# Kernel optimization log

Measured on AMD Instinct MI355X. Metric: run time of the kernel, lower is better.

## Reference

```python
import jax, jax.numpy as jnp
import numpy as np

TAU = 0.02
M = 5  # len(modality_types) + 1; modality 0 == padding


def setup_inputs() -> dict:
    B, Q, S, D = 64, 32, 256, 128
    key = jax.random.key(0)
    k0, k1, k2, k3, k4 = jax.random.split(key, 5)
    q = jax.random.normal(k0, (B, Q, D), dtype=jnp.float32)
    q = q / jnp.linalg.norm(q, axis=-1, keepdims=True)
    d = jax.random.normal(k1, (B, S, D), dtype=jnp.float32)
    d = d / jnp.linalg.norm(d, axis=-1, keepdims=True)
    # guarantee every modality 0..M-1 appears in each doc (first M tokens)
    head = jnp.tile(jnp.arange(M, dtype=jnp.int32), (B, 1))
    rest = jax.random.randint(k2, (B, S - M), 0, M, dtype=jnp.int32)
    modality_ids = jnp.concatenate([head, rest], axis=1)
    query_types = jax.random.randint(k3, (B,), 1, M, dtype=jnp.int32)  # in [1, M-1]
    lengths = jax.random.randint(k4, (B,), Q // 2, Q + 1)
    query_mask = jnp.arange(Q)[None, :] < lengths[:, None]
    return {"query_emb": q, "doc_emb": d, "modality_ids": modality_ids,
            "query_types": query_types, "query_mask": query_mask}


def _loss(query_emb, doc_emb, modality_ids, query_types, query_mask):
    B = query_emb.shape[0]
    idx = jnp.arange(B)
    # token-level similarity: (B, C, Q, S)
    base = jnp.einsum('bqd,csd->bcqs', query_emb, doc_emb)
    qnorm = jnp.maximum(query_mask.sum(axis=1), 1).astype(base.dtype)  # (B,)

    # agg (ColBERT max-sim): max over non-pad doc tokens, masked query sum
    nonpad = (modality_ids != 0)[None, :, None, :]
    agg_max = jnp.where(nonpad, base, -jnp.inf).max(axis=-1)           # (B, C, Q)
    sim = (agg_max * query_mask[:, None, :].astype(base.dtype)).sum(axis=-1)
    sim = sim / qnorm[:, None]                                          # (B, C)

    # _all_modality_sims: segmented max over s per modality, then sum over q
    per_mod = []
    for m in range(M):
        mask_m = (modality_ids == m)[None, :, None, :]
        per_mod.append(jnp.where(mask_m, base, -jnp.inf).max(axis=-1).sum(axis=-1))
    sims = jnp.stack(per_mod, axis=-1)                                  # (B, C, M)
    sims = sims / qnorm[:, None, None]

    # replace diagonal with the query's own modality score
    sim_fixed = sim.at[idx, idx].set(sims[idx, idx, query_types])

    # hard negatives: all (doc, modality) pairs except pad modality and own positive
    all_modal = sims.reshape(B, B * M)
    keep_mask = jnp.ones((B, B * M), dtype=bool)
    keep_mask = keep_mask.at[:, 0::M].set(False)
    keep_mask = keep_mask.at[idx, idx * M + query_types].set(False)
    n_keep = B * M - B - 1  # exact per-row count (query_types >= 1, no overlap)
    order = jnp.argsort((~keep_mask).astype(jnp.int32), axis=1, stable=True)[:, :n_keep]
    extras = jnp.take_along_axis(all_modal, order, axis=1)              # (B, n_keep)

    logits = jnp.concatenate([sim_fixed, extras], axis=1) / TAU
    # cross entropy with labels = arange(B) (positive is column b)
    return (jax.nn.logsumexp(logits, axis=1) - logits[idx, idx]).mean()


def reference(query_emb, doc_emb, modality_ids, query_types, query_mask):
    return _loss(query_emb, doc_emb, modality_ids, query_types, query_mask)
```

## Files before the change

### kernel.cpp

```cpp
#include <hip/hip_runtime.h>
#include <math.h>

#define TAU_F 0.02f
#define NB 64
#define NQ 32
#define NS 256
#define ND 128
#define MAXT 12
#define PERMSTRIDE 384

typedef __bf16 bf16x8 __attribute__((ext_vector_type(8)));
typedef float f32x16 __attribute__((ext_vector_type(16)));

#define OFF_TILEMOD 0u
#define OFF_TCOUNT  4096u
#define OFF_DFRAG   16384u
#define OFF_QFRAG   6307840u
#define OFF_SIMOUT  6832128u
#define OFF_RED     6914048u

__global__ __launch_bounds__(256) void
prep_frag_kernel(const float* __restrict__ qemb, const float* __restrict__ demb,
                 const int* __restrict__ mod,
                 __bf16* __restrict__ qfrag, __bf16* __restrict__ dfrag,
                 int* __restrict__ tilemod_g, int* __restrict__ tcount_g,
                 int* __restrict__ red) {
    int blk = blockIdx.x;
    int tid = threadIdx.x;
    int lane = tid & 63, wv = tid >> 6;
    int li32 = lane & 31, kh = lane >> 5;

    if (blk == 0 && tid == 0) { red[0] = 0; ((float*)red)[16] = 0.f; }

    if (blk >= NB) {
        int b = blk - NB;
#pragma unroll
        for (int i = 0; i < 2; ++i) {
            int kc = wv * 2 + i;
            int k0 = kc * 16 + kh * 8;
            const float* src = qemb + ((size_t)b * NQ + li32) * ND + k0;
            float4 a = *(const float4*)src;
            float4 bq = *(const float4*)(src + 4);
            bf16x8 o;
            o[0] = (__bf16)a.x;  o[1] = (__bf16)a.y;  o[2] = (__bf16)a.z;  o[3] = (__bf16)a.w;
            o[4] = (__bf16)bq.x; o[5] = (__bf16)bq.y; o[6] = (__bf16)bq.z; o[7] = (__bf16)bq.w;
            *(bf16x8*)(qfrag + (((size_t)b * 8 + kc) * 64 + lane) * 8) = o;
        }
        return;
    }

    int c = blk;
    __shared__ int smod[NS];
    __shared__ int sperm[PERMSTRIDE];
    __shared__ int counts[5], firsts[5], offs[5], padded[5];
    __shared__ int stilemod[MAXT];
    __shared__ int sT;

    if (tid < 5) { counts[tid] = 0; firsts[tid] = NS; }
    __syncthreads();
    int m_tok = mod[c * NS + tid];
    smod[tid] = m_tok;
    if (m_tok) { atomicAdd(&counts[m_tok], 1); atomicMin(&firsts[m_tok], tid); }
    __syncthreads();
    if (tid == 0) {
        int pos = 0;
        for (int m = 1; m <= 4; ++m) {
            offs[m] = pos;
            int p = (counts[m] + 31) & ~31;
            padded[m] = p;
            for (int t = pos >> 5; t < (pos + p) >> 5; ++t) stilemod[t] = m;
            pos += p;
        }
        sT = pos >> 5;
        tcount_g[c] = pos >> 5;
    }
    __syncthreads();
    if (m_tok) {
        int rank = 0;
        for (int s = 0; s < tid; ++s) rank += (smod[s] == m_tok);
        sperm[offs[m_tok] + rank] = tid;
    }
    if (tid < 4) {
        int m = tid + 1;
        for (int p = counts[m]; p < padded[m]; ++p) sperm[offs[m] + p] = firsts[m];
    }
    __syncthreads();
    int T = sT;
    if (tid < T) tilemod_g[c * MAXT + tid] = stilemod[tid];

    for (int kc = wv; kc < 8; kc += 4) {
        int k0 = kc * 16 + kh * 8;
        for (int t = 0; t < T; ++t) {
            int srow = sperm[t * 32 + li32];
            const float* src = demb + ((size_t)c * NS + srow) * ND + k0;
            float4 a = *(const float4*)src;
            float4 bq = *(const float4*)(src + 4);
            bf16x8 o;
            o[0] = (__bf16)a.x;  o[1] = (__bf16)a.y;  o[2] = (__bf16)a.z;  o[3] = (__bf16)a.w;
            o[4] = (__bf16)bq.x; o[5] = (__bf16)bq.y; o[6] = (__bf16)bq.z; o[7] = (__bf16)bq.w;
            *(bf16x8*)(dfrag + (((size_t)(c * MAXT + t) * 8 + kc) * 64 + lane) * 8) = o;
        }
    }
}

__global__ __launch_bounds__(256, 2) void
main_kernel(const __bf16* __restrict__ dfrag, const __bf16* __restrict__ qfrag,
            const int* __restrict__ tilemod, const int* __restrict__ tcount,
            const int* __restrict__ qmask, float* __restrict__ simout) {
    int blk = blockIdx.x;
    int xcd = blk & 7;
    int idx = blk >> 3;
    int c   = xcd * 8 + (idx & 7);
    int bq  = idx >> 3;
    int tid = threadIdx.x;
    int lane = tid & 63, wv = tid >> 6;
    int b0 = bq * 8 + wv * 2;

    bf16x8 bfrag[2][8];
#pragma unroll
    for (int bi = 0; bi < 2; ++bi)
#pragma unroll
        for (int kc = 0; kc < 8; ++kc)
            bfrag[bi][kc] = *(const bf16x8*)(qfrag + (((size_t)(b0 + bi) * 8 + kc) * 64 + lane) * 8);

    __shared__ __bf16 sbuf[2][8 * 64 * 8];

    int T = tcount[c];
    const __bf16* dbase = dfrag + (size_t)c * MAXT * 4096;

    {
        const __bf16* src = dbase;
        *(bf16x8*)&sbuf[0][(size_t)tid * 8]          = *(const bf16x8*)(src + (size_t)tid * 8);
        *(bf16x8*)&sbuf[0][2048 + (size_t)tid * 8]   = *(const bf16x8*)(src + 2048 + (size_t)tid * 8);
    }
    __syncthreads();

    float vmax[2][4];
#pragma unroll
    for (int bi = 0; bi < 2; ++bi)
#pragma unroll
        for (int m = 0; m < 4; ++m) vmax[bi][m] = -1e30f;

    int cur = 0;
    for (int t = 0; t < T; ++t) {
        bf16x8 p0, p1;
        bool pf = (t + 1 < T);
        if (pf) {
            const __bf16* src = dbase + (size_t)(t + 1) * 4096;
            p0 = *(const bf16x8*)(src + (size_t)tid * 8);
            p1 = *(const bf16x8*)(src + 2048 + (size_t)tid * 8);
        }

        int tm = tilemod[c * MAXT + t];
        f32x16 acc0 = {0.f,0.f,0.f,0.f,0.f,0.f,0.f,0.f,0.f,0.f,0.f,0.f,0.f,0.f,0.f,0.f};
        f32x16 acc1 = acc0;
#pragma unroll
        for (int kc = 0; kc < 8; ++kc) {
            bf16x8 af = *(const bf16x8*)&sbuf[cur][(kc * 64 + lane) * 8];
            acc0 = __builtin_amdgcn_mfma_f32_32x32x16_bf16(af, bfrag[0][kc], acc0, 0, 0, 0);
            acc1 = __builtin_amdgcn_mfma_f32_32x32x16_bf16(af, bfrag[1][kc], acc1, 0, 0, 0);
        }
        float v0 = acc0[0], v1 = acc1[0];
#pragma unroll
        for (int r = 1; r < 16; ++r) { v0 = fmaxf(v0, acc0[r]); v1 = fmaxf(v1, acc1[r]); }
        v0 = fmaxf(v0, __shfl_xor(v0, 32, 64));
        v1 = fmaxf(v1, __shfl_xor(v1, 32, 64));
        switch (tm) {
        case 1:  vmax[0][0] = fmaxf(vmax[0][0], v0); vmax[1][0] = fmaxf(vmax[1][0], v1); break;
        case 2:  vmax[0][1] = fmaxf(vmax[0][1], v0); vmax[1][1] = fmaxf(vmax[1][1], v1); break;
        case 3:  vmax[0][2] = fmaxf(vmax[0][2], v0); vmax[1][2] = fmaxf(vmax[1][2], v1); break;
        default: vmax[0][3] = fmaxf(vmax[0][3], v0); vmax[1][3] = fmaxf(vmax[1][3], v1); break;
        }

        if (pf) {
            *(bf16x8*)&sbuf[cur ^ 1][(size_t)tid * 8]        = p0;
            *(bf16x8*)&sbuf[cur ^ 1][2048 + (size_t)tid * 8] = p1;
        }
        __syncthreads();
        cur ^= 1;
    }

    int q = lane & 31;
#pragma unroll
    for (int bi = 0; bi < 2; ++bi) {
        int b = b0 + bi;
        float m1 = vmax[bi][0], m2 = vmax[bi][1], m3 = vmax[bi][2], m4 = vmax[bi][3];
        float agg = fmaxf(fmaxf(m1, m2), fmaxf(m3, m4));
        float s0 = (qmask[b * NQ + q] != 0) ? agg : 0.f;
        float s1 = m1, s2 = m2, s3 = m3, s4 = m4;
#pragma unroll
        for (int off = 16; off >= 1; off >>= 1) {
            s0 += __shfl_xor(s0, off, 64);
            s1 += __shfl_xor(s1, off, 64);
            s2 += __shfl_xor(s2, off, 64);
            s3 += __shfl_xor(s3, off, 64);
            s4 += __shfl_xor(s4, off, 64);
        }
        if (lane == 0) {
            float* o = simout + ((size_t)b * NB + c) * 5;
            o[0] = s0; o[1] = s1; o[2] = s2; o[3] = s3; o[4] = s4;
        }
    }
}

__global__ __launch_bounds__(256) void
loss_kernel(const float* __restrict__ simout, const int* __restrict__ qtypes,
            const int* __restrict__ qmask, int* __restrict__ red,
            float* __restrict__ out) {
    int r = blockIdx.x;
    int tid = threadIdx.x;
    int lane = tid & 63, wv = tid >> 6;

    __shared__ float sv[320];
    for (int i = tid; i < 320; i += 256) sv[i] = simout[(size_t)r * 320 + i];

    __shared__ int scnt;
    if (wv == 0) {
        int on = (lane < NQ) ? (qmask[r * NQ + lane] != 0) : 0;
        unsigned long long bal = __ballot(on);
        if (lane == 0) scnt = __popcll(bal);
    }
    __syncthreads();
    int cq = scnt;
    float scale = 1.0f / (TAU_F * (float)(cq > 0 ? cq : 1));
    int skip = r * 5;

    __shared__ float wred[4];
    float mx = -1e30f;
    for (int i = tid; i < 320; i += 256)
        if (i != skip) mx = fmaxf(mx, sv[i] * scale);
#pragma unroll
    for (int off = 32; off >= 1; off >>= 1) mx = fmaxf(mx, __shfl_xor(mx, off, 64));
    if (lane == 0) wred[wv] = mx;
    __syncthreads();
    mx = fmaxf(fmaxf(wred[0], wred[1]), fmaxf(wred[2], wred[3]));

    float sum = 0.f;
    for (int i = tid; i < 320; i += 256)
        if (i != skip) sum += expf(sv[i] * scale - mx);
#pragma unroll
    for (int off = 32; off >= 1; off >>= 1) sum += __shfl_xor(sum, off, 64);
    __syncthreads();
    if (lane == 0) wred[wv] = sum;
    __syncthreads();

    if (tid == 0) {
        float tot = wred[0] + wred[1] + wred[2] + wred[3];
        float pos = sv[r * 5 + qtypes[r]] * scale;
        float lr = (logf(tot) + mx - pos) * (1.0f / NB);
        float* acc = (float*)red + 16;
        float ret = atomicAdd(acc, lr);
        int bump = 1 + (ret > 1e37f ? 1 : 0);
        int old = atomicAdd(red, bump);
        if (old == NB - 1) {
            float v = atomicAdd(acc, 0.f);
            out[0] = v;
        }
    }
}

extern "C" void kernel_launch(void* const* d_in, const int* in_sizes, int n_in,
                              void* d_out, int out_size, void* d_ws, size_t ws_size,
                              hipStream_t stream) {
    const float* qemb   = (const float*)d_in[0];
    const float* demb   = (const float*)d_in[1];
    const int*   mod    = (const int*)d_in[2];
    const int*   qtypes = (const int*)d_in[3];
    const int*   qmask  = (const int*)d_in[4];

    char* ws = (char*)d_ws;
    int*    tilemod = (int*)(ws + OFF_TILEMOD);
    int*    tcount  = (int*)(ws + OFF_TCOUNT);
    __bf16* dfrag   = (__bf16*)(ws + OFF_DFRAG);
    __bf16* qfrag   = (__bf16*)(ws + OFF_QFRAG);
    float*  simout  = (float*)(ws + OFF_SIMOUT);
    int*    red     = (int*)(ws + OFF_RED);

    prep_frag_kernel<<<2 * NB, 256, 0, stream>>>(qemb, demb, mod, qfrag, dfrag,
                                                 tilemod, tcount, red);
    main_kernel<<<512, 256, 0, stream>>>(dfrag, qfrag, tilemod, tcount, qmask, simout);
    loss_kernel<<<NB, 256, 0, stream>>>(simout, qtypes, qmask, red, (float*)d_out);
}
```

Measured before the change: 91.51 us.

## Fuse bf16 fragment prep and modality sorting into the main MFMA kernel

```diff
diff --git a/kernel.cpp b/kernel.cpp
--- a/kernel.cpp
+++ b/kernel.cpp
@@ -12,101 +12,20 @@
 typedef __bf16 bf16x8 __attribute__((ext_vector_type(8)));
 typedef float f32x16 __attribute__((ext_vector_type(16)));
 
-#define OFF_TILEMOD 0u
-#define OFF_TCOUNT  4096u
-#define OFF_DFRAG   16384u
-#define OFF_QFRAG   6307840u
-#define OFF_SIMOUT  6832128u
-#define OFF_RED     6914048u
-
-__global__ __launch_bounds__(256) void
-prep_frag_kernel(const float* __restrict__ qemb, const float* __restrict__ demb,
-                 const int* __restrict__ mod,
-                 __bf16* __restrict__ qfrag, __bf16* __restrict__ dfrag,
-                 int* __restrict__ tilemod_g, int* __restrict__ tcount_g,
-                 int* __restrict__ red) {
-    int blk = blockIdx.x;
-    int tid = threadIdx.x;
-    int lane = tid & 63, wv = tid >> 6;
-    int li32 = lane & 31, kh = lane >> 5;
-
-    if (blk == 0 && tid == 0) { red[0] = 0; ((float*)red)[16] = 0.f; }
-
-    if (blk >= NB) {
-        int b = blk - NB;
-#pragma unroll
-        for (int i = 0; i < 2; ++i) {
-            int kc = wv * 2 + i;
-            int k0 = kc * 16 + kh * 8;
-            const float* src = qemb + ((size_t)b * NQ + li32) * ND + k0;
-            float4 a = *(const float4*)src;
-            float4 bq = *(const float4*)(src + 4);
-            bf16x8 o;
-            o[0] = (__bf16)a.x;  o[1] = (__bf16)a.y;  o[2] = (__bf16)a.z;  o[3] = (__bf16)a.w;
-            o[4] = (__bf16)bq.x; o[5] = (__bf16)bq.y; o[6] = (__bf16)bq.z; o[7] = (__bf16)bq.w;
-            *(bf16x8*)(qfrag + (((size_t)b * 8 + kc) * 64 + lane) * 8) = o;
-        }
-        return;
-    }
-
-    int c = blk;
-    __shared__ int smod[NS];
-    __shared__ int sperm[PERMSTRIDE];
-    __shared__ int counts[5], firsts[5], offs[5], padded[5];
-    __shared__ int stilemod[MAXT];
-    __shared__ int sT;
-
-    if (tid < 5) { counts[tid] = 0; firsts[tid] = NS; }
-    __syncthreads();
-    int m_tok = mod[c * NS + tid];
-    smod[tid] = m_tok;
-    if (m_tok) { atomicAdd(&counts[m_tok], 1); atomicMin(&firsts[m_tok], tid); }
-    __syncthreads();
-    if (tid == 0) {
-        int pos = 0;
-        for (int m = 1; m <= 4; ++m) {
-            offs[m] = pos;
-            int p = (counts[m] + 31) & ~31;
-            padded[m] = p;
-            for (int t = pos >> 5; t < (pos + p) >> 5; ++t) stilemod[t] = m;
-            pos += p;
-        }
-        sT = pos >> 5;
-        tcount_g[c] = pos >> 5;
-    }
-    __syncthreads();
-    if (m_tok) {
-        int rank = 0;
-        for (int s = 0; s < tid; ++s) rank += (smod[s] == m_tok);
-        sperm[offs[m_tok] + rank] = tid;
-    }
-    if (tid < 4) {
-        int m = tid + 1;
-        for (int p = counts[m]; p < padded[m]; ++p) sperm[offs[m] + p] = firsts[m];
-    }
-    __syncthreads();
-    int T = sT;
-    if (tid < T) tilemod_g[c * MAXT + tid] = stilemod[tid];
-
-    for (int kc = wv; kc < 8; kc += 4) {
-        int k0 = kc * 16 + kh * 8;
-        for (int t = 0; t < T; ++t) {
-            int srow = sperm[t * 32 + li32];
-            const float* src = demb + ((size_t)c * NS + srow) * ND + k0;
-            float4 a = *(const float4*)src;
-            float4 bq = *(const float4*)(src + 4);
-            bf16x8 o;
-            o[0] = (__bf16)a.x;  o[1] = (__bf16)a.y;  o[2] = (__bf16)a.z;  o[3] = (__bf16)a.w;
-            o[4] = (__bf16)bq.x; o[5] = (__bf16)bq.y; o[6] = (__bf16)bq.z; o[7] = (__bf16)bq.w;
-            *(bf16x8*)(dfrag + (((size_t)(c * MAXT + t) * 8 + kc) * 64 + lane) * 8) = o;
-        }
-    }
+#define OFF_SIMOUT 0u
+#define OFF_RED    81920u
+
+__device__ inline bf16x8 cvt2(float4 a, float4 b) {
+    bf16x8 o;
+    o[0] = (__bf16)a.x; o[1] = (__bf16)a.y; o[2] = (__bf16)a.z; o[3] = (__bf16)a.w;
+    o[4] = (__bf16)b.x; o[5] = (__bf16)b.y; o[6] = (__bf16)b.z; o[7] = (__bf16)b.w;
+    return o;
 }
 
 __global__ __launch_bounds__(256, 2) void
-main_kernel(const __bf16* __restrict__ dfrag, const __bf16* __restrict__ qfrag,
-            const int* __restrict__ tilemod, const int* __restrict__ tcount,
-            const int* __restrict__ qmask, float* __restrict__ simout) {
+main_kernel(const float* __restrict__ qemb, const float* __restrict__ demb,
+            const int* __restrict__ mod, const int* __restrict__ qmask,
+            float* __restrict__ simout, int* __restrict__ red) {
     int blk = blockIdx.x;
     int xcd = blk & 7;
     int idx = blk >> 3;
@@ -114,24 +33,75 @@
     int bq  = idx >> 3;
     int tid = threadIdx.x;
     int lane = tid & 63, wv = tid >> 6;
+    int li32 = lane & 31, kh = lane >> 5;
     int b0 = bq * 8 + wv * 2;
 
+    if (blk == 0 && tid == 0) { red[0] = 0; ((float*)red)[16] = 0.f; }
+
     bf16x8 bfrag[2][8];
 #pragma unroll
     for (int bi = 0; bi < 2; ++bi)
 #pragma unroll
-        for (int kc = 0; kc < 8; ++kc)
-            bfrag[bi][kc] = *(const bf16x8*)(qfrag + (((size_t)(b0 + bi) * 8 + kc) * 64 + lane) * 8);
+        for (int kc = 0; kc < 8; ++kc) {
+            const float* src = qemb + ((size_t)(b0 + bi) * NQ + li32) * ND + kc * 16 + kh * 8;
+            float4 a = *(const float4*)src;
+            float4 b = *(const float4*)(src + 4);
+            bfrag[bi][kc] = cvt2(a, b);
+        }
+
+    __shared__ int sperm[PERMSTRIDE];
+    __shared__ int wcnt[4][4];
+    __shared__ int counts[5], firsts[5], offs[5], padded[5];
+    __shared__ int stilemod[MAXT];
+    __shared__ int sT;
+
+    int m_tok = mod[c * NS + tid];
+    int rank_w = 0;
+#pragma unroll
+    for (int m = 1; m <= 4; ++m) {
+        unsigned long long bal = __ballot(m_tok == m);
+        if (lane == 0) wcnt[wv][m - 1] = __popcll(bal);
+        if (m_tok == m) rank_w = __popcll(bal & ((1ull << lane) - 1ull));
+    }
+    __syncthreads();
+    if (tid == 0) {
+        int pos = 0;
+        for (int m = 1; m <= 4; ++m) {
+            int cnt = wcnt[0][m-1] + wcnt[1][m-1] + wcnt[2][m-1] + wcnt[3][m-1];
+            counts[m] = cnt;
+            offs[m] = pos;
+            int p = (cnt + 31) & ~31;
+            padded[m] = p;
+            for (int t = pos >> 5; t < (pos + p) >> 5; ++t) stilemod[t] = m;
+            pos += p;
+        }
+        sT = pos >> 5;
+    }
+    __syncthreads();
+    if (m_tok) {
+        int rank = rank_w;
+        for (int w = 0; w < wv; ++w) rank += wcnt[w][m_tok - 1];
+        sperm[offs[m_tok] + rank] = tid;
+        if (rank == 0) firsts[m_tok] = tid;
+    }
+    __syncthreads();
+    if (tid < 4) {
+        int m = tid + 1;
+        for (int p = counts[m]; p < padded[m]; ++p) sperm[offs[m] + p] = firsts[m];
+    }
+    __syncthreads();
+    int T = sT;
 
     __shared__ __bf16 sbuf[2][8 * 64 * 8];
-
-    int T = tcount[c];
-    const __bf16* dbase = dfrag + (size_t)c * MAXT * 4096;
+    int row = tid & 31, chunk = tid >> 5;
+    const float* drow_base = demb + (size_t)c * NS * ND + chunk * 16;
 
     {
-        const __bf16* src = dbase;
-        *(bf16x8*)&sbuf[0][(size_t)tid * 8]          = *(const bf16x8*)(src + (size_t)tid * 8);
-        *(bf16x8*)&sbuf[0][2048 + (size_t)tid * 8]   = *(const bf16x8*)(src + 2048 + (size_t)tid * 8);
+        int srow = sperm[row];
+        const float4* s = (const float4*)(drow_base + (size_t)srow * ND);
+        float4 a0 = s[0], a1 = s[1], a2 = s[2], a3 = s[3];
+        *(bf16x8*)&sbuf[0][((chunk * 64) + row) * 8]      = cvt2(a0, a1);
+        *(bf16x8*)&sbuf[0][((chunk * 64) + 32 + row) * 8] = cvt2(a2, a3);
     }
     __syncthreads();
 
@@ -143,15 +113,15 @@
 
     int cur = 0;
     for (int t = 0; t < T; ++t) {
-        bf16x8 p0, p1;
+        float4 a0, a1, a2, a3;
         bool pf = (t + 1 < T);
         if (pf) {
-            const __bf16* src = dbase + (size_t)(t + 1) * 4096;
-            p0 = *(const bf16x8*)(src + (size_t)tid * 8);
-            p1 = *(const bf16x8*)(src + 2048 + (size_t)tid * 8);
-        }
-
-        int tm = tilemod[c * MAXT + t];
+            int srow = sperm[(t + 1) * 32 + row];
+            const float4* s = (const float4*)(drow_base + (size_t)srow * ND);
+            a0 = s[0]; a1 = s[1]; a2 = s[2]; a3 = s[3];
+        }
+
+        int tm = stilemod[t];
         f32x16 acc0 = {0.f,0.f,0.f,0.f,0.f,0.f,0.f,0.f,0.f,0.f,0.f,0.f,0.f,0.f,0.f,0.f};
         f32x16 acc1 = acc0;
 #pragma unroll
@@ -160,9 +130,16 @@
             acc0 = __builtin_amdgcn_mfma_f32_32x32x16_bf16(af, bfrag[0][kc], acc0, 0, 0, 0);
             acc1 = __builtin_amdgcn_mfma_f32_32x32x16_bf16(af, bfrag[1][kc], acc1, 0, 0, 0);
         }
-        float v0 = acc0[0], v1 = acc1[0];
-#pragma unroll
-        for (int r = 1; r < 16; ++r) { v0 = fmaxf(v0, acc0[r]); v1 = fmaxf(v1, acc1[r]); }
+        float v0 = fmaxf(fmaxf(fmaxf(acc0[0], acc0[1]),  fmaxf(acc0[2],  acc0[3])),
+                         fmaxf(fmaxf(acc0[4], acc0[5]),  fmaxf(acc0[6],  acc0[7])));
+        v0 = fmaxf(v0,
+             fmaxf(fmaxf(fmaxf(acc0[8], acc0[9]),  fmaxf(acc0[10], acc0[11])),
+                   fmaxf(fmaxf(acc0[12], acc0[13]), fmaxf(acc0[14], acc0[15]))));
+        float v1 = fmaxf(fmaxf(fmaxf(acc1[0], acc1[1]),  fmaxf(acc1[2],  acc1[3])),
+                         fmaxf(fmaxf(acc1[4], acc1[5]),  fmaxf(acc1[6],  acc1[7])));
+        v1 = fmaxf(v1,
+             fmaxf(fmaxf(fmaxf(acc1[8], acc1[9]),  fmaxf(acc1[10], acc1[11])),
+                   fmaxf(fmaxf(acc1[12], acc1[13]), fmaxf(acc1[14], acc1[15]))));
         v0 = fmaxf(v0, __shfl_xor(v0, 32, 64));
         v1 = fmaxf(v1, __shfl_xor(v1, 32, 64));
         switch (tm) {
@@ -173,8 +150,8 @@
         }
 
         if (pf) {
-            *(bf16x8*)&sbuf[cur ^ 1][(size_t)tid * 8]        = p0;
-            *(bf16x8*)&sbuf[cur ^ 1][2048 + (size_t)tid * 8] = p1;
+            *(bf16x8*)&sbuf[cur ^ 1][((chunk * 64) + row) * 8]      = cvt2(a0, a1);
+            *(bf16x8*)&sbuf[cur ^ 1][((chunk * 64) + 32 + row) * 8] = cvt2(a2, a3);
         }
         __syncthreads();
         cur ^= 1;
@@ -269,15 +246,9 @@
     const int*   qmask  = (const int*)d_in[4];
 
     char* ws = (char*)d_ws;
-    int*    tilemod = (int*)(ws + OFF_TILEMOD);
-    int*    tcount  = (int*)(ws + OFF_TCOUNT);
-    __bf16* dfrag   = (__bf16*)(ws + OFF_DFRAG);
-    __bf16* qfrag   = (__bf16*)(ws + OFF_QFRAG);
-    float*  simout  = (float*)(ws + OFF_SIMOUT);
-    int*    red     = (int*)(ws + OFF_RED);
-
-    prep_frag_kernel<<<2 * NB, 256, 0, stream>>>(qemb, demb, mod, qfrag, dfrag,
-                                                 tilemod, tcount, red);
-    main_kernel<<<512, 256, 0, stream>>>(dfrag, qfrag, tilemod, tcount, qmask, simout);
+    float* simout = (float*)(ws + OFF_SIMOUT);
+    int*   red    = (int*)(ws + OFF_RED);
+
+    main_kernel<<<512, 256, 0, stream>>>(qemb, demb, mod, qmask, simout, red);
     loss_kernel<<<NB, 256, 0, stream>>>(simout, qtypes, qmask, red, (float*)d_out);
 }
```

After: 93.07 us. No clear change (+1.7%).
